# Kernel tuning notes

Measured on AMD Instinct MI355X. Metric: run time of the kernel, lower is better.

## Reference

```python
import jax, jax.numpy as jnp
import numpy as np

B, T = 64, 512
OBS, DM, DS, NL = 115, 128, 8, 3
EMB, NA, H1 = 16, 19, 256


def _ln(x, g, b, eps=1e-5):
    m = jnp.mean(x, -1, keepdims=True)
    v = jnp.mean((x - m) ** 2, -1, keepdims=True)
    return (x - m) * jax.lax.rsqrt(v + eps) * g + b


def _s6(x, h, lng, lnb, w_ig, w_dt, b_dt, a_log, w_b, w_c, d_par, w_out):
    # x: [B,T,DM], h: [B,DM,DS]
    xn = _ln(x, lng, lnb)
    xp = xn @ w_ig.T                               # [B,T,2*DM]
    x_in, z = xp[..., :DM], xp[..., DM:]
    dt = jax.nn.softplus(x_in @ w_dt.T + b_dt)     # [B,T,DM]
    A = -jnp.exp(a_log)                            # [DM,DS]
    bt = x_in @ w_b.T                              # [B,T,DS]
    ct = x_in @ w_c.T                              # [B,T,DS]
    dA = jnp.exp(dt[..., None] * A)                # [B,T,DM,DS]
    upd = (dt * x_in)[..., None] * bt[:, :, None, :]  # [B,T,DM,DS]

    def step(hc, inp):
        dA_t, u_t, c_t = inp
        hn = dA_t * hc + u_t                       # [B,DM,DS]
        y = jnp.einsum('bds,bs->bd', hn, c_t)      # [B,DM]
        return hn, y

    h_f, ys = jax.lax.scan(
        step, h,
        (jnp.swapaxes(dA, 0, 1), jnp.swapaxes(upd, 0, 1), jnp.swapaxes(ct, 0, 1)))
    y = jnp.swapaxes(ys, 0, 1)                     # [B,T,DM]
    ssm = y * jax.nn.silu(z) + x_in * d_par
    return x + ssm @ w_out.T, h_f.reshape(h_f.shape[0], -1)


def _forward(prev_actions, obs, h0, enc_w1, enc_b1, enc_g1, enc_bb1, enc_w2, enc_b2,
             enc_g2, enc_bb2, emb, proj_w, proj_b, proj_g, proj_bb,
             m_ln_g, m_ln_b, m_w_ig, m_w_dt, m_b_dt, m_a_log, m_w_b, m_w_c, m_d, m_w_out,
             fn_g, fn_b, pol_w1, pol_b1, pol_g, pol_bb, pol_w2, pol_b2):
    # MLP encoder: Linear -> LN -> SiLU -> Linear -> LN (final norm)
    e = jax.nn.silu(_ln(obs @ enc_w1.T + enc_b1, enc_g1, enc_bb1))
    e = _ln(e @ enc_w2.T + enc_b2, enc_g2, enc_bb2)
    pa = emb[prev_actions]                         # [B,T,EMB]
    x = jnp.concatenate([e, pa], -1) @ proj_w.T + proj_b
    x = jax.nn.silu(_ln(x, proj_g, proj_bb))
    for i in range(NL):
        x, _ = _s6(x, h0[i].reshape(-1, DM, DS), m_ln_g[i], m_ln_b[i], m_w_ig[i],
                   m_w_dt[i], m_b_dt[i], m_a_log[i], m_w_b[i], m_w_c[i], m_d[i], m_w_out[i])
    x = _ln(x, fn_g, fn_b)
    p = jax.nn.silu(_ln(x @ pol_w1.T + pol_b1, pol_g, pol_bb))
    return p @ pol_w2.T + pol_b2                   # [B,T,NA] policy logits


def setup_inputs() -> dict:
    key = jax.random.key(0)
    ks = iter(jax.random.split(key, 64))
    def n(shape, s=0.05):
        return jax.random.normal(next(ks), shape, dtype=jnp.float32) * s
    return {
        'obs': jax.random.normal(next(ks), (B, T, OBS), dtype=jnp.float32),
        'h0': jnp.zeros((NL, B, DM * DS), jnp.float32),
        'enc_w1': n((H1, OBS)), 'enc_b1': jnp.zeros((H1,)),
        'enc_g1': jnp.ones((H1,)), 'enc_bb1': jnp.zeros((H1,)),
        'enc_w2': n((DM, H1)), 'enc_b2': jnp.zeros((DM,)),
        'enc_g2': jnp.ones((DM,)), 'enc_bb2': jnp.zeros((DM,)),
        'emb': n((NA + 1, EMB), 1.0),
        'proj_w': n((DM, DM + EMB)), 'proj_b': jnp.zeros((DM,)),
        'proj_g': jnp.ones((DM,)), 'proj_bb': jnp.zeros((DM,)),
        'm_ln_g': jnp.ones((NL, DM)), 'm_ln_b': jnp.zeros((NL, DM)),
        'm_w_ig': n((NL, 2 * DM, DM)), 'm_w_dt': n((NL, DM, DM)),
        'm_b_dt': jnp.zeros((NL, DM)),
        'm_a_log': jax.random.uniform(next(ks), (NL, DM, DS), minval=-3.0, maxval=-1.0, dtype=jnp.float32),
        'm_w_b': n((NL, DS, DM)), 'm_w_c': n((NL, DS, DM)),
        'm_d': jnp.ones((NL, DM)), 'm_w_out': n((NL, DM, DM)),
        'fn_g': jnp.ones((DM,)), 'fn_b': jnp.zeros((DM,)),
        'pol_w1': n((DM, DM)), 'pol_b1': jnp.zeros((DM,)),
        'pol_g': jnp.ones((DM,)), 'pol_bb': jnp.zeros((DM,)),
        'pol_w2': n((NA, DM)), 'pol_b2': jnp.zeros((NA,)),
        'prev_actions': jax.random.randint(next(ks), (B, T), 0, NA + 1),
    }


def reference(obs, h0, enc_w1, enc_b1, enc_g1, enc_bb1, enc_w2, enc_b2, enc_g2, enc_bb2,
              emb, proj_w, proj_b, proj_g, proj_bb, m_ln_g, m_ln_b, m_w_ig, m_w_dt,
              m_b_dt, m_a_log, m_w_b, m_w_c, m_d, m_w_out, fn_g, fn_b, pol_w1, pol_b1,
              pol_g, pol_bb, pol_w2, pol_b2, prev_actions):
    return _forward(prev_actions, obs, h0, enc_w1, enc_b1, enc_g1, enc_bb1, enc_w2,
                    enc_b2, enc_g2, enc_bb2, emb, proj_w, proj_b, proj_g, proj_bb,
                    m_ln_g, m_ln_b, m_w_ig, m_w_dt, m_b_dt, m_a_log, m_w_b, m_w_c,
                    m_d, m_w_out, fn_g, fn_b, pol_w1, pol_b1, pol_g, pol_bb, pol_w2, pol_b2)
```

## Files before the change

### kernel.cpp

```cpp
#include <hip/hip_runtime.h>
#include <math.h>

#define BB 64
#define TT 512
#define OBSD 115
#define DMD 128
#define DSD 8
#define NLD 3
#define EMBD 16
#define NAD 19
#define H1D 256
#define NTOK (BB*TT)
#define SSEG 32
#define TSEG (TT/SSEG)

typedef unsigned short ushort_t;
typedef __attribute__((ext_vector_type(8))) short short8;
typedef __attribute__((ext_vector_type(4))) float f32x4;

__device__ __forceinline__ float silu_f(float x){ return x / (1.f + __expf(-x)); }
__device__ __forceinline__ float softplus_f(float x){
  return fmaxf(x, 0.f) + log1pf(__expf(-fabsf(x)));
}
__device__ __forceinline__ ushort_t f2bf(float x){
  unsigned u = __float_as_uint(x);
  unsigned r = (u + 0x7fffu + ((u >> 16) & 1u)) >> 16;
  return (ushort_t)r;
}
__device__ __forceinline__ float b2f(ushort_t x){
  return __uint_as_float(((unsigned)x) << 16);
}
#define MFMA(a,b,c) __builtin_amdgcn_mfma_f32_16x16x32_bf16((a),(b),(c),0,0,0)
#define LOG2E 1.44269504f

template<int D, int SV>
__device__ __forceinline__ void ln32(const float* s_val, float* s_mr, int tid){
  const int t = tid >> 3, part = tid & 7;
  float s = 0.f, s2 = 0.f;
  #pragma unroll
  for (int j = part; j < D; j += 8){ float v = s_val[t*SV + j]; s += v; s2 = fmaf(v, v, s2); }
  s += __shfl_xor(s, 1, 64); s2 += __shfl_xor(s2, 1, 64);
  s += __shfl_xor(s, 2, 64); s2 += __shfl_xor(s2, 2, 64);
  s += __shfl_xor(s, 4, 64); s2 += __shfl_xor(s2, 4, 64);
  if (part == 0){
    float m = s * (1.f/(float)D);
    s_mr[t*2] = m;
    s_mr[t*2+1] = rsqrtf(s2 * (1.f/(float)D) - m*m + 1e-5f);
  }
}

struct PJob { const float* src; ushort_t* dst; int N; int K; int Kpad; int rowofs; int Nw; };
struct PJobs { PJob j[20]; };

__global__ __launch_bounds__(256) void k_prep(PJobs P){
  const int job = blockIdx.x >> 2;
  const int sub = blockIdx.x & 3;
  PJob pj = P.j[job];
  const int elems = pj.Nw * pj.Kpad;
  for (int idx = sub*256 + threadIdx.x; idx < elems; idx += 4*256){
    int n = idx / pj.Kpad;
    int k = idx - n*pj.Kpad;
    float v = (n < pj.N && k < pj.K) ? pj.src[(size_t)n*pj.K + k] : 0.f;
    pj.dst[(size_t)(pj.rowofs + n)*pj.Kpad + k] = f2bf(v);
  }
}

__global__ __launch_bounds__(256) void k_enc12p(
    const float* __restrict__ obs, const ushort_t* __restrict__ w1b,
    const float* __restrict__ b1, const float* __restrict__ g1,
    const float* __restrict__ bb1,
    const ushort_t* __restrict__ w2b,
    const float* __restrict__ b2, const float* __restrict__ g2,
    const float* __restrict__ bb2,
    const float* __restrict__ emb, const int* __restrict__ pact,
    const ushort_t* __restrict__ pwb, const float* __restrict__ pb,
    const float* __restrict__ pg, const float* __restrict__ pbb,
    float* __restrict__ X,
    const float* __restrict__ lng, const float* __restrict__ lnb,
    const ushort_t* __restrict__ wigb, const ushort_t* __restrict__ wdbcb,
    const float* __restrict__ bdt,
    ushort_t* __restrict__ XINb, ushort_t* __restrict__ Zb,
    ushort_t* __restrict__ DTb, ushort_t* __restrict__ BTu, ushort_t* __restrict__ CTu,
    const float* __restrict__ alog0,
    float* __restrict__ HLOC, float* __restrict__ PPR)
{
  __shared__ __align__(16) char sm[35584];
  float*    s_val  = (float*)sm;
  ushort_t* s_obs  = (ushort_t*)sm;
  ushort_t* s_xin  = (ushort_t*)sm;
  ushort_t* s_dt   = (ushort_t*)(sm + 8704);
  ushort_t* s_e1   = (ushort_t*)(sm + 17408);
  ushort_t* s_a2   = (ushort_t*)(sm + 17408);
  float2*   s_st   = (float2*)(sm + 34304);
  ushort_t* s_btc  = (ushort_t*)(sm + 34816);
  float*    s_mr   = (float*)(sm + 35328);

  const int tok0 = blockIdx.x * 32;
  const int bidx = blockIdx.x >> 4;
  const int ch   = blockIdx.x & 15;
  const int tid = threadIdx.x;
  const int lane = tid & 63, w = tid >> 6;
  const int q = lane >> 4, cn = lane & 15;
  const int m0 = (w & 1) * 16, nh = w >> 1;

  for (int e = tid; e < 32*16; e += 256){
    int t = e >> 4, kc = e & 15;
    const float* op = obs + (size_t)(tok0 + t)*OBSD;
    short8 v;
    #pragma unroll
    for (int j = 0; j < 8; j++){
      int k = kc*8 + j;
      v[j] = (short)f2bf(k < OBSD ? op[k] : 0.f);
    }
    *(short8*)&s_obs[t*136 + kc*8] = v;
  }
  __syncthreads();

  f32x4 acc[8];
  {
    short8 af[4];
    #pragma unroll
    for (int ks = 0; ks < 4; ks++)
      af[ks] = *(const short8*)&s_obs[(m0 + cn)*136 + ks*32 + q*8];
    #pragma unroll
    for (int nt = 0; nt < 8; nt++){
      const int n0 = (nh*8 + nt) * 16;
      f32x4 a = {0.f,0.f,0.f,0.f};
      #pragma unroll
      for (int ks = 0; ks < 4; ks++){
        short8 bf = *(const short8*)&w1b[(size_t)(n0 + cn)*128 + ks*32 + q*8];
        a = MFMA(af[ks], bf, a);
      }
      float bv = b1[n0 + cn];
      #pragma unroll
      for (int r = 0; r < 4; r++) a[r] += bv;
      acc[nt] = a;
    }
  }

  {
    #pragma unroll
    for (int r = 0; r < 4; r++){
      float s = 0.f, s2 = 0.f;
      #pragma unroll
      for (int nt = 0; nt < 8; nt++){ float v = acc[nt][r]; s += v; s2 = fmaf(v, v, s2); }
      s += __shfl_xor(s, 1, 64); s2 += __shfl_xor(s2, 1, 64);
      s += __shfl_xor(s, 2, 64); s2 += __shfl_xor(s2, 2, 64);
      s += __shfl_xor(s, 4, 64); s2 += __shfl_xor(s2, 4, 64);
      s += __shfl_xor(s, 8, 64); s2 += __shfl_xor(s2, 8, 64);
      if (cn == 0) s_st[(m0 + q*4 + r)*2 + nh] = make_float2(s, s2);
    }
  }
  __syncthreads();

  {
    float mu[4], rs[4];
    #pragma unroll
    for (int r = 0; r < 4; r++){
      const int row = m0 + q*4 + r;
      float2 p0 = s_st[row*2 + 0], p1 = s_st[row*2 + 1];
      float s = p0.x + p1.x, s2 = p0.y + p1.y;
      float m = s * (1.f/256.f);
      mu[r] = m;
      rs[r] = rsqrtf(s2 * (1.f/256.f) - m*m + 1e-5f);
    }
    #pragma unroll
    for (int nt = 0; nt < 8; nt++){
      const int col = (nh*8 + nt)*16 + cn;
      float gg = g1[col], bbv = bb1[col];
      #pragma unroll
      for (int r = 0; r < 4; r++){
        float v = (acc[nt][r] - mu[r]) * rs[r] * gg + bbv;
        s_e1[(m0 + q*4 + r)*264 + col] = f2bf(silu_f(v));
      }
    }
  }
  __syncthreads();

  {
    short8 af2[8];
    #pragma unroll
    for (int ks = 0; ks < 8; ks++)
      af2[ks] = *(const short8*)&s_e1[(m0 + cn)*264 + ks*32 + q*8];
    __syncthreads();

    for (int e = tid; e < 32*32; e += 256){
      int t = e >> 5, k = e & 31;
      float v = 0.f;
      if (k < EMBD){ int a = pact[tok0 + t]; v = emb[(size_t)a*EMBD + k]; }
      s_a2[t*168 + 128 + k] = f2bf(v);
    }

    #pragma unroll
    for (int nt = 0; nt < 4; nt++){
      const int n0 = (nh*4 + nt) * 16;
      f32x4 a = {0.f,0.f,0.f,0.f};
      #pragma unroll
      for (int ks = 0; ks < 8; ks++){
        short8 bf = *(const short8*)&w2b[(size_t)(n0 + cn)*256 + ks*32 + q*8];
        a = MFMA(af2[ks], bf, a);
      }
      float bias = b2[n0 + cn];
      #pragma unroll
      for (int r = 0; r < 4; r++)
        s_val[(m0 + q*4 + r)*136 + n0 + cn] = a[r] + bias;
    }
  }
  __syncthreads();

  ln32<128,136>(s_val, s_mr, tid);
  __syncthreads();
  for (int e = tid; e < 32*128; e += 256){
    int t = e >> 7, c = e & 127;
    float v = (s_val[t*136 + c] - s_mr[t*2]) * s_mr[t*2+1] * g2[c] + bb2[c];
    s_a2[t*168 + c] = f2bf(v);
  }
  __syncthreads();

  {
    short8 af3[5];
    #pragma unroll
    for (int ks = 0; ks < 5; ks++)
      af3[ks] = *(const short8*)&s_a2[(m0 + cn)*168 + ks*32 + q*8];
    #pragma unroll
    for (int nt = 0; nt < 4; nt++){
      const int n0 = (nh*4 + nt) * 16;
      f32x4 a = {0.f,0.f,0.f,0.f};
      #pragma unroll
      for (int ks = 0; ks < 5; ks++){
        short8 bf = *(const short8*)&pwb[(size_t)(n0 + cn)*160 + ks*32 + q*8];
        a = MFMA(af3[ks], bf, a);
      }
      float bias = pb[n0 + cn];
      #pragma unroll
      for (int r = 0; r < 4; r++)
        s_val[(m0 + q*4 + r)*136 + n0 + cn] = a[r] + bias;
    }
  }
  __syncthreads();

  ln32<128,136>(s_val, s_mr, tid);
  __syncthreads();
  for (int e = tid; e < 32*128; e += 256){
    int t = e >> 7, c = e & 127;
    float v = (s_val[t*136 + c] - s_mr[t*2]) * s_mr[t*2+1] * pg[c] + pbb[c];
    v = silu_f(v);
    X[(size_t)tok0*128 + e] = v;
    s_val[t*136 + c] = v;
  }
  __syncthreads();

  ln32<128,136>(s_val, s_mr, tid);
  __syncthreads();
  for (int e = tid; e < 32*128; e += 256){
    int t = e >> 7, c = e & 127;
    float v = (s_val[t*136 + c] - s_mr[t*2]) * s_mr[t*2+1] * lng[c] + lnb[c];
    s_a2[t*168 + c] = f2bf(v);
  }
  __syncthreads();

  {
    short8 af[4];
    #pragma unroll
    for (int ks = 0; ks < 4; ks++)
      af[ks] = *(const short8*)&s_a2[(m0 + cn)*168 + ks*32 + q*8];
    #pragma unroll
    for (int nt = 0; nt < 8; nt++){
      const int n0 = (nh*8 + nt) * 16;
      f32x4 a = {0.f,0.f,0.f,0.f};
      #pragma unroll
      for (int ks = 0; ks < 4; ks++){
        short8 bf = *(const short8*)&wigb[(size_t)(n0 + cn)*128 + ks*32 + q*8];
        a = MFMA(af[ks], bf, a);
      }
      if (n0 < 128){
        #pragma unroll
        for (int r = 0; r < 4; r++){
          int tr = m0 + q*4 + r;
          ushort_t bb = f2bf(a[r]);
          XINb[(size_t)(tok0 + tr)*128 + n0 + cn] = bb;
          s_xin[tr*136 + n0 + cn] = bb;
        }
      } else {
        #pragma unroll
        for (int r = 0; r < 4; r++){
          int tr = m0 + q*4 + r;
          Zb[(size_t)(tok0 + tr)*128 + (n0 - 128) + cn] = f2bf(a[r]);
        }
      }
    }
  }
  __syncthreads();

  {
    short8 af2[4];
    #pragma unroll
    for (int ks = 0; ks < 4; ks++)
      af2[ks] = *(const short8*)&s_xin[(m0 + cn)*136 + ks*32 + q*8];
    for (int nt = nh; nt < 9; nt += 2){
      const int n0 = nt * 16;
      f32x4 a = {0.f,0.f,0.f,0.f};
      #pragma unroll
      for (int ks = 0; ks < 4; ks++){
        short8 bf = *(const short8*)&wdbcb[(size_t)(n0 + cn)*128 + ks*32 + q*8];
        a = MFMA(af2[ks], bf, a);
      }
      const int col = n0 + cn;
      if (col < 128){
        float bd = bdt[col];
        #pragma unroll
        for (int r = 0; r < 4; r++){
          int tr = m0 + q*4 + r;
          ushort_t dv = f2bf(softplus_f(a[r] + bd));
          DTb[(size_t)(tok0 + tr)*128 + col] = dv;
          s_dt[tr*136 + col] = dv;
        }
      } else if (col < 136){
        #pragma unroll
        for (int r = 0; r < 4; r++){
          int tr = m0 + q*4 + r;
          ushort_t bb = f2bf(a[r]);
          BTu[(size_t)(tok0 + tr)*8 + (col - 128)] = bb;
          s_btc[tr*8 + (col - 128)] = bb;
        }
      } else {
        #pragma unroll
        for (int r = 0; r < 4; r++)
          CTu[(size_t)(tok0 + m0 + q*4 + r)*8 + (col - 136)] = f2bf(a[r]);
      }
    }
  }
  __syncthreads();

  {
    const int d = tid & 127, half = tid >> 7;
    float A2c[8], hh[8], pp[8];
    #pragma unroll
    for (int s = 0; s < 8; s++){
      A2c[s] = -__expf(alog0[d*8 + s]) * LOG2E;
      hh[s] = 0.f; pp[s] = 1.f;
    }
    const int t0 = half * 16;
    #pragma unroll 4
    for (int tt = 0; tt < 16; tt++){
      const int t = t0 + tt;
      float dt = b2f(s_dt[t*136 + d]);
      float wv = dt * b2f(s_xin[t*136 + d]);
      #pragma unroll
      for (int s = 0; s < 8; s++){
        float dA = exp2f(dt * A2c[s]);
        hh[s] = fmaf(dA, hh[s], wv * b2f(s_btc[t*8 + s]));
        pp[s] *= dA;
      }
    }
    const size_t o = ((size_t)bidx*SSEG + ch*2 + half)*1024 + d*8;
    #pragma unroll
    for (int s = 0; s < 8; s++){ HLOC[o+s] = hh[s]; PPR[o+s] = pp[s]; }
  }
}

__global__ __launch_bounds__(256) void k_carry(
    float* __restrict__ HL, const float* __restrict__ PP,
    const float* __restrict__ h0g)
{
  const int idx = blockIdx.x*256 + threadIdx.x;
  const size_t base = (size_t)(idx >> 10) * (SSEG*1024) + (idx & 1023);
  float hl[SSEG], pp[SSEG];
  #pragma unroll
  for (int ch = 0; ch < SSEG; ch++){
    hl[ch] = HL[base + (size_t)ch*1024];
    pp[ch] = PP[base + (size_t)ch*1024];
  }
  float h = h0g[idx];
  #pragma unroll
  for (int ch = 0; ch < SSEG; ch++){
    HL[base + (size_t)ch*1024] = h;
    h = fmaf(pp[ch], h, hl[ch]);
  }
}

#define SMB 26624

__device__ __forceinline__ void phaseB32(
    const ushort_t* DTb, const ushort_t* XINb, const ushort_t* Zb,
    const ushort_t* BTu, const ushort_t* CTu,
    const float* __restrict__ alog, const float* __restrict__ HLpre,
    const float* __restrict__ dpar, const ushort_t* __restrict__ woutb,
    float* __restrict__ X, char* sm, int b, int pair, int tid)
{
  ushort_t* s_dtS = (ushort_t*)sm;
  ushort_t* s_xiS = (ushort_t*)(sm + 8192);
  float*    s_x   = (float*)sm;
  ushort_t* s_a   = (ushort_t*)(sm + 16640);
  ushort_t* s_bt  = (ushort_t*)(sm + 25344);
  ushort_t* s_ct  = (ushort_t*)(sm + 25856);
  float*    s_mr  = (float*)(sm + 26368);

  const int lane = tid & 63, w = tid >> 6, q = lane >> 4, cn = lane & 15;
  const int m0 = (w & 1) * 16, nh = w >> 1;
  const int d = tid & 127, half = tid >> 7;
  const size_t segtok = (size_t)b*TT + pair*32;

  {
    const uint4* gdt = (const uint4*)(DTb + segtok*128);
    const uint4* gxi = (const uint4*)(XINb + segtok*128);
    #pragma unroll
    for (int i = 0; i < 2; i++){
      ((uint4*)s_dtS)[tid + i*256] = gdt[tid + i*256];
      ((uint4*)s_xiS)[tid + i*256] = gxi[tid + i*256];
    }
    if (tid < 128){
      ((unsigned*)s_bt)[tid] = ((const unsigned*)(BTu + segtok*8))[tid];
      ((unsigned*)s_ct)[tid] = ((const unsigned*)(CTu + segtok*8))[tid];
    }
  }
  float A2[8], h[8];
  {
    const size_t o = ((size_t)b*SSEG + pair*2 + half)*1024 + d*8;
    float4 h0v = *(const float4*)(HLpre + o);
    float4 h1v = *(const float4*)(HLpre + o + 4);
    h[0]=h0v.x; h[1]=h0v.y; h[2]=h0v.z; h[3]=h0v.w;
    h[4]=h1v.x; h[5]=h1v.y; h[6]=h1v.z; h[7]=h1v.w;
    #pragma unroll
    for (int s = 0; s < 8; s++) A2[s] = -__expf(alog[d*8 + s]) * LOG2E;
  }
  __syncthreads();

  #pragma unroll 4
  for (int tt = 0; tt < 16; tt++){
    const int t = half*16 + tt;
    float dt = b2f(s_dtS[t*128 + d]);
    float xi = b2f(s_xiS[t*128 + d]);
    float wv = dt * xi;
    float y = 0.f;
    #pragma unroll
    for (int s = 0; s < 8; s++){
      float dA = exp2f(dt * A2[s]);
      h[s] = fmaf(dA, h[s], wv * b2f(s_bt[t*8 + s]));
      y = fmaf(h[s], b2f(s_ct[t*8 + s]), y);
    }
    s_a[t*136 + d] = f2bf(y);
  }
  __syncthreads();

  {
    const int c0 = (tid & 15)*8, trow = tid >> 4;
    float dpv[8];
    #pragma unroll
    for (int j = 0; j < 8; j++) dpv[j] = dpar[c0 + j];
    #pragma unroll
    for (int i = 0; i < 2; i++){
      const int t = trow + i*16;
      uint4 zb = ((const uint4*)(Zb + segtok*128))[tid + i*256];
      const ushort_t* zp = (const ushort_t*)&zb;
      #pragma unroll
      for (int j = 0; j < 8; j++){
        float y  = b2f(s_a[t*136 + c0 + j]);
        float xi = b2f(s_xiS[t*128 + c0 + j]);
        float ssm = y * silu_f(b2f(zp[j])) + xi * dpv[j];
        s_a[t*136 + c0 + j] = f2bf(ssm);
      }
    }
  }
  __syncthreads();

  {
    short8 af[4];
    #pragma unroll
    for (int ks = 0; ks < 4; ks++)
      af[ks] = *(const short8*)&s_a[(m0 + cn)*136 + ks*32 + q*8];
    #pragma unroll
    for (int i = 0; i < 4; i++){
      const int n0 = (nh*4 + i) * 16;
      short8 bf[4];
      #pragma unroll
      for (int ks = 0; ks < 4; ks++)
        bf[ks] = *(const short8*)&woutb[(size_t)(n0+cn)*128 + ks*32 + q*8];
      f32x4 acc = {0.f,0.f,0.f,0.f};
      #pragma unroll
      for (int ks = 0; ks < 4; ks++) acc = MFMA(af[ks], bf[ks], acc);
      #pragma unroll
      for (int r = 0; r < 4; r++){
        const int tr = m0 + q*4 + r;
        const size_t g = (segtok + tr)*128 + n0 + cn;
        float xn = X[g] + acc[r];
        X[g] = xn;
        s_x[tr*130 + n0 + cn] = xn;
      }
    }
  }
  __syncthreads();

  {
    const int t = tid >> 3, part = tid & 7;
    float s = 0.f, s2 = 0.f;
    const float* row = s_x + t*130 + part*16;
    #pragma unroll
    for (int j = 0; j < 16; j++){ float v = row[j]; s += v; s2 = fmaf(v, v, s2); }
    s  += __shfl_xor(s, 1, 64);  s2 += __shfl_xor(s2, 1, 64);
    s  += __shfl_xor(s, 2, 64);  s2 += __shfl_xor(s2, 2, 64);
    s  += __shfl_xor(s, 4, 64);  s2 += __shfl_xor(s2, 4, 64);
    if (part == 0){
      float m = s * (1.f/128.f);
      s_mr[t*2] = m;
      s_mr[t*2+1] = rsqrtf(s2 * (1.f/128.f) - m*m + 1e-5f);
    }
  }
  __syncthreads();
}

__global__ __launch_bounds__(256, 4) void k_scan2p(
    ushort_t* DTb, ushort_t* XINb, ushort_t* Zb,
    ushort_t* BTu, ushort_t* CTu,
    const float* __restrict__ alog, const float* __restrict__ HLpre,
    const float* __restrict__ dpar, const ushort_t* __restrict__ woutb,
    float* __restrict__ X,
    const float* __restrict__ lng, const float* __restrict__ lnb,
    const ushort_t* __restrict__ wigb, const ushort_t* __restrict__ wdbcb,
    const float* __restrict__ bdt,
    const float* __restrict__ alogn,
    float* __restrict__ HLo, float* __restrict__ PPo)
{
  __shared__ __align__(16) char sm[SMB];
  const int tid = threadIdx.x;
  float*    s_x   = (float*)sm;
  ushort_t* s_xin = (ushort_t*)sm;
  ushort_t* s_dt2 = (ushort_t*)(sm + 8704);
  ushort_t* s_a   = (ushort_t*)(sm + 16640);
  ushort_t* s_btc = (ushort_t*)(sm + 25344);
  float*    s_mr  = (float*)(sm + 26368);

  const int b = blockIdx.x >> 4;
  const int pair = blockIdx.x & 15;
  const int lane = tid & 63, w = tid >> 6, q = lane >> 4, cn = lane & 15;
  const int m0 = (w & 1) * 16, nh = w >> 1;
  const int d = tid & 127, half = tid >> 7;
  const size_t segtok = (size_t)b*TT + pair*32;

  phaseB32(DTb, XINb, Zb, BTu, CTu, alog, HLpre, dpar, woutb, X, sm, b, pair, tid);

  {
    float g = lng[d], c0v = lnb[d];
    #pragma unroll
    for (int tt = 0; tt < 16; tt++){
      const int t = half*16 + tt;
      float v = (s_x[t*130 + d] - s_mr[t*2]) * s_mr[t*2+1] * g + c0v;
      s_a[t*136 + d] = f2bf(v);
    }
  }
  __syncthreads();

  {
    short8 af[4];
    #pragma unroll
    for (int ks = 0; ks < 4; ks++)
      af[ks] = *(const short8*)&s_a[(m0 + cn)*136 + ks*32 + q*8];
    #pragma unroll
    for (int i = 0; i < 8; i++){
      const int n0 = (nh*8 + i) * 16;
      short8 bf[4];
      #pragma unroll
      for (int ks = 0; ks < 4; ks++)
        bf[ks] = *(const short8*)&wigb[(size_t)(n0+cn)*128 + ks*32 + q*8];
      f32x4 acc = {0.f,0.f,0.f,0.f};
      #pragma unroll
      for (int ks = 0; ks < 4; ks++) acc = MFMA(af[ks], bf[ks], acc);
      if (n0 < 128){
        #pragma unroll
        for (int r = 0; r < 4; r++){
          const int tr = m0 + q*4 + r;
          ushort_t bb = f2bf(acc[r]);
          XINb[(segtok + tr)*128 + n0 + cn] = bb;
          s_xin[tr*136 + n0 + cn] = bb;
        }
      } else {
        #pragma unroll
        for (int r = 0; r < 4; r++){
          const int tr = m0 + q*4 + r;
          Zb[(segtok + tr)*128 + (n0-128) + cn] = f2bf(acc[r]);
        }
      }
    }
  }
  __syncthreads();

  {
    short8 af2[4];
    #pragma unroll
    for (int ks = 0; ks < 4; ks++)
      af2[ks] = *(const short8*)&s_xin[(m0 + cn)*136 + ks*32 + q*8];
    for (int nt = nh; nt < 9; nt += 2){
      const int n0 = nt * 16;
      short8 bf[4];
      #pragma unroll
      for (int ks = 0; ks < 4; ks++)
        bf[ks] = *(const short8*)&wdbcb[(size_t)(n0+cn)*128 + ks*32 + q*8];
      f32x4 acc = {0.f,0.f,0.f,0.f};
      #pragma unroll
      for (int ks = 0; ks < 4; ks++) acc = MFMA(af2[ks], bf[ks], acc);
      const int col = n0 + cn;
      if (col < 128){
        float bd = bdt[col];
        #pragma unroll
        for (int r = 0; r < 4; r++){
          const int tr = m0 + q*4 + r;
          ushort_t dv = f2bf(softplus_f(acc[r] + bd));
          DTb[(segtok + tr)*128 + col] = dv;
          s_dt2[tr*136 + col] = dv;
        }
      } else if (col < 136){
        #pragma unroll
        for (int r = 0; r < 4; r++){
          const int tr = m0 + q*4 + r;
          ushort_t bb = f2bf(acc[r]);
          BTu[(segtok + tr)*8 + (col-128)] = bb;
          s_btc[tr*8 + (col-128)] = bb;
        }
      } else {
        #pragma unroll
        for (int r = 0; r < 4; r++)
          CTu[(segtok + m0 + q*4 + r)*8 + (col-136)] = f2bf(acc[r]);
      }
    }
  }
  __syncthreads();

  {
    float A2n[8], hh[8], pp[8];
    #pragma unroll
    for (int s = 0; s < 8; s++){
      A2n[s] = -__expf(alogn[d*8 + s]) * LOG2E;
      hh[s] = 0.f; pp[s] = 1.f;
    }
    #pragma unroll 4
    for (int tt = 0; tt < 16; tt++){
      const int t = half*16 + tt;
      float dt = b2f(s_dt2[t*136 + d]);
      float wv = dt * b2f(s_xin[t*136 + d]);
      #pragma unroll
      for (int s = 0; s < 8; s++){
        float dA = exp2f(dt * A2n[s]);
        hh[s] = fmaf(dA, hh[s], wv * b2f(s_btc[t*8 + s]));
        pp[s] *= dA;
      }
    }
    const size_t o = ((size_t)b*SSEG + pair*2 + half)*1024 + d*8;
    #pragma unroll
    for (int s = 0; s < 8; s++){ HLo[o+s] = hh[s]; PPo[o+s] = pp[s]; }
  }
}

__global__ __launch_bounds__(256, 4) void k_scan2h(
    const ushort_t* DTb, const ushort_t* XINb, const ushort_t* Zb,
    const ushort_t* BTu, const ushort_t* CTu,
    const float* __restrict__ alog, const float* __restrict__ HLpre,
    const float* __restrict__ dpar, const ushort_t* __restrict__ woutb,
    float* __restrict__ X,
    const float* __restrict__ fng, const float* __restrict__ fnb,
    const ushort_t* __restrict__ pw1b, const float* __restrict__ pb1,
    const float* __restrict__ pg, const float* __restrict__ pbb,
    const ushort_t* __restrict__ pw2b, const float* __restrict__ pb2,
    float* __restrict__ out)
{
  __shared__ __align__(16) char sm[SMB];
  const int tid = threadIdx.x;
  float*    s_x  = (float*)sm;
  ushort_t* s_a  = (ushort_t*)(sm + 16640);
  float*    s_mr = (float*)(sm + 26368);

  const int b = blockIdx.x >> 4;
  const int pair = blockIdx.x & 15;
  const int lane = tid & 63, w = tid >> 6, q = lane >> 4, cn = lane & 15;
  const int m0 = (w & 1) * 16, nh = w >> 1;
  const int d = tid & 127, half = tid >> 7;
  const size_t segtok = (size_t)b*TT + pair*32;

  phaseB32((ushort_t*)DTb, (ushort_t*)XINb, (ushort_t*)Zb,
           (ushort_t*)BTu, (ushort_t*)CTu, alog, HLpre,
           dpar, woutb, X, sm, b, pair, tid);

  {
    float g = fng[d], c0v = fnb[d];
    #pragma unroll
    for (int tt = 0; tt < 16; tt++){
      const int t = half*16 + tt;
      float v = (s_x[t*130 + d] - s_mr[t*2]) * s_mr[t*2+1] * g + c0v;
      s_a[t*136 + d] = f2bf(v);
    }
  }
  __syncthreads();

  {
    short8 af[4];
    #pragma unroll
    for (int ks = 0; ks < 4; ks++)
      af[ks] = *(const short8*)&s_a[(m0 + cn)*136 + ks*32 + q*8];
    #pragma unroll
    for (int i = 0; i < 4; i++){
      const int n0 = (nh*4 + i) * 16;
      short8 bf[4];
      #pragma unroll
      for (int ks = 0; ks < 4; ks++)
        bf[ks] = *(const short8*)&pw1b[(size_t)(n0+cn)*128 + ks*32 + q*8];
      float bias = pb1[n0 + cn];
      f32x4 acc = {0.f,0.f,0.f,0.f};
      #pragma unroll
      for (int ks = 0; ks < 4; ks++) acc = MFMA(af[ks], bf[ks], acc);
      #pragma unroll
      for (int r = 0; r < 4; r++)
        s_x[(m0 + q*4 + r)*130 + n0 + cn] = acc[r] + bias;
    }
  }
  __syncthreads();

  {
    const int t = tid >> 3, part = tid & 7;
    float s = 0.f, s2 = 0.f;
    const float* row = s_x + t*130 + part*16;
    #pragma unroll
    for (int j = 0; j < 16; j++){ float v = row[j]; s += v; s2 = fmaf(v, v, s2); }
    s  += __shfl_xor(s, 1, 64);  s2 += __shfl_xor(s2, 1, 64);
    s  += __shfl_xor(s, 2, 64);  s2 += __shfl_xor(s2, 2, 64);
    s  += __shfl_xor(s, 4, 64);  s2 += __shfl_xor(s2, 4, 64);
    if (part == 0){
      float m = s * (1.f/128.f);
      s_mr[t*2] = m;
      s_mr[t*2+1] = rsqrtf(s2 * (1.f/128.f) - m*m + 1e-5f);
    }
  }
  __syncthreads();

  {
    float g = pg[d], c0v = pbb[d];
    #pragma unroll
    for (int tt = 0; tt < 16; tt++){
      const int t = half*16 + tt;
      float v = (s_x[t*130 + d] - s_mr[t*2]) * s_mr[t*2+1] * g + c0v;
      s_a[t*136 + d] = f2bf(silu_f(v));
    }
  }
  __syncthreads();

  {
    short8 af[4];
    #pragma unroll
    for (int ks = 0; ks < 4; ks++)
      af[ks] = *(const short8*)&s_a[(m0 + cn)*136 + ks*32 + q*8];
    const int n0 = (w >> 1) * 16;
    short8 bf[4];
    #pragma unroll
    for (int ks = 0; ks < 4; ks++)
      bf[ks] = *(const short8*)&pw2b[(size_t)(n0+cn)*128 + ks*32 + q*8];
    const int col = n0 + cn;
    f32x4 acc = {0.f,0.f,0.f,0.f};
    #pragma unroll
    for (int ks = 0; ks < 4; ks++) acc = MFMA(af[ks], bf[ks], acc);
    if (col < NAD){
      float bias = pb2[col];
      #pragma unroll
      for (int r = 0; r < 4; r++)
        out[(segtok + m0 + q*4 + r)*NAD + col] = acc[r] + bias;
    }
  }
}

extern "C" void kernel_launch(void* const* d_in, const int* in_sizes, int n_in,
                              void* d_out, int out_size, void* d_ws, size_t ws_size,
                              hipStream_t stream) {
  const float* obs    = (const float*)d_in[0];
  const float* h0     = (const float*)d_in[1];
  const float* enc_w1 = (const float*)d_in[2];
  const float* enc_b1 = (const float*)d_in[3];
  const float* enc_g1 = (const float*)d_in[4];
  const float* enc_bb1= (const float*)d_in[5];
  const float* enc_w2 = (const float*)d_in[6];
  const float* enc_b2 = (const float*)d_in[7];
  const float* enc_g2 = (const float*)d_in[8];
  const float* enc_bb2= (const float*)d_in[9];
  const float* emb    = (const float*)d_in[10];
  const float* proj_w = (const float*)d_in[11];
  const float* proj_b = (const float*)d_in[12];
  const float* proj_g = (const float*)d_in[13];
  const float* proj_bb= (const float*)d_in[14];
  const float* m_ln_g = (const float*)d_in[15];
  const float* m_ln_b = (const float*)d_in[16];
  const float* m_w_ig = (const float*)d_in[17];
  const float* m_w_dt = (const float*)d_in[18];
  const float* m_b_dt = (const float*)d_in[19];
  const float* m_a_log= (const float*)d_in[20];
  const float* m_w_b  = (const float*)d_in[21];
  const float* m_w_c  = (const float*)d_in[22];
  const float* m_d    = (const float*)d_in[23];
  const float* m_w_out= (const float*)d_in[24];
  const float* fn_g   = (const float*)d_in[25];
  const float* fn_b   = (const float*)d_in[26];
  const float* pol_w1 = (const float*)d_in[27];
  const float* pol_b1 = (const float*)d_in[28];
  const float* pol_g  = (const float*)d_in[29];
  const float* pol_bb = (const float*)d_in[30];
  const float* pol_w2 = (const float*)d_in[31];
  const float* pol_b2 = (const float*)d_in[32];
  const int*   pact   = (const int*)d_in[33];

  float* ws  = (float*)d_ws;
  float* X    = ws;
  float* HLA  = X + (size_t)NTOK*128;
  float* PPA  = HLA + (size_t)BB*SSEG*1024;
  float* HLB  = PPA + (size_t)BB*SSEG*1024;
  float* PPB  = HLB + (size_t)BB*SSEG*1024;
  ushort_t* XINb = (ushort_t*)(PPB + (size_t)BB*SSEG*1024);
  ushort_t* Zb   = XINb + (size_t)NTOK*128;
  ushort_t* DTb  = Zb   + (size_t)NTOK*128;
  ushort_t* BTu  = DTb  + (size_t)NTOK*128;
  ushort_t* CTu  = BTu  + (size_t)NTOK*8;

  ushort_t* W1B   = CTu   + (size_t)NTOK*8;
  ushort_t* W2B   = W1B   + 256*128;
  ushort_t* PWB   = W2B   + 128*256;
  ushort_t* WIGB  = PWB   + 128*160;
  ushort_t* WDBCB = WIGB  + 3*256*128;
  ushort_t* WOUTB = WDBCB + 3*144*128;
  ushort_t* PW1B  = WOUTB + 3*128*128;
  ushort_t* PW2B  = PW1B  + 128*128;

  PJobs P;
  int nj = 0;
  auto add = [&](const float* src, ushort_t* dst, int N, int K, int Kpad, int rowofs, int Nw){
    P.j[nj].src = src; P.j[nj].dst = dst; P.j[nj].N = N; P.j[nj].K = K;
    P.j[nj].Kpad = Kpad; P.j[nj].rowofs = rowofs; P.j[nj].Nw = Nw; nj++;
  };
  add(enc_w1, W1B, 256, 115, 128, 0, 256);
  add(enc_w2, W2B, 128, 256, 256, 0, 128);
  add(proj_w, PWB, 128, 144, 160, 0, 128);
  for (int l = 0; l < NLD; l++)
    add(m_w_ig + (size_t)l*256*128, WIGB + (size_t)l*256*128, 256, 128, 128, 0, 256);
  for (int l = 0; l < NLD; l++){
    add(m_w_dt + (size_t)l*128*128, WDBCB + (size_t)l*144*128, 128, 128, 128, 0,   128);
    add(m_w_b  + (size_t)l*8*128,   WDBCB + (size_t)l*144*128,   8, 128, 128, 128,   8);
    add(m_w_c  + (size_t)l*8*128,   WDBCB + (size_t)l*144*128,   8, 128, 128, 136,   8);
  }
  for (int l = 0; l < NLD; l++)
    add(m_w_out + (size_t)l*128*128, WOUTB + (size_t)l*128*128, 128, 128, 128, 0, 128);
  add(pol_w1, PW1B, 128, 128, 128, 0, 128);
  add(pol_w2, PW2B,  19, 128, 128, 0,  32);

  k_prep<<<20*4, 256, 0, stream>>>(P);
  k_enc12p<<<NTOK/32, 256, 0, stream>>>(obs, W1B, enc_b1, enc_g1, enc_bb1,
      W2B, enc_b2, enc_g2, enc_bb2,
      emb, pact, PWB, proj_b, proj_g, proj_bb, X,
      m_ln_g, m_ln_b, WIGB, WDBCB, m_b_dt,
      XINb, Zb, DTb, BTu, CTu,
      m_a_log, HLA, PPA);

  const int carrygrid = BB*1024/256;
  const int scangrid  = NTOK/32;

  k_carry<<<carrygrid, 256, 0, stream>>>(HLA, PPA, h0);
  k_scan2p<<<scangrid, 256, 0, stream>>>(DTb, XINb, Zb, BTu, CTu,
      m_a_log, HLA, m_d, WOUTB, X,
      m_ln_g + 128, m_ln_b + 128,
      WIGB + (size_t)256*128, WDBCB + (size_t)144*128, m_b_dt + 128,
      m_a_log + 1024, HLB, PPB);
  k_carry<<<carrygrid, 256, 0, stream>>>(HLB, PPB, h0 + (size_t)BB*1024);
  k_scan2p<<<scangrid, 256, 0, stream>>>(DTb, XINb, Zb, BTu, CTu,
      m_a_log + 1024, HLB, m_d + 128, WOUTB + (size_t)128*128, X,
      m_ln_g + 256, m_ln_b + 256,
      WIGB + (size_t)2*256*128, WDBCB + (size_t)2*144*128, m_b_dt + 256,
      m_a_log + 2048, HLA, PPA);
  k_carry<<<carrygrid, 256, 0, stream>>>(HLA, PPA, h0 + (size_t)2*BB*1024);
  k_scan2h<<<scangrid, 256, 0, stream>>>(DTb, XINb, Zb, BTu, CTu,
      m_a_log + 2048, HLA, m_d + 256, WOUTB + (size_t)2*128*128, X,
      fn_g, fn_b, PW1B, pol_b1, pol_g, pol_bb, PW2B, pol_b2,
      (float*)d_out);
}
```

Before: 409.0 us.

## Fuse LayerNorm statistics into MFMA epilogues and merge SSM gating into scan

LayerNorm mean/variance is now reduced from the MFMA accumulator registers with lane shuffles and cross-wave partials in shared memory. This replaces the separate shared-memory store, reduce pass and normalize pass, removing several barriers and LDS round trips in the encoder and scan kernels. The z gate and D-skip are now applied inside the scan loop, with z preloaded into shared memory, instead of in a separate pass that re-read y and x_in. In exchange the shared-memory footprint of the scan kernels grows, which may lower occupancy, and the encoder gets a launch-bounds occupancy hint.

```diff
diff --git a/kernel.cpp b/kernel.cpp
--- a/kernel.cpp
+++ b/kernel.cpp
@@ -33,22 +33,6 @@
 #define MFMA(a,b,c) __builtin_amdgcn_mfma_f32_16x16x32_bf16((a),(b),(c),0,0,0)
 #define LOG2E 1.44269504f
 
-template<int D, int SV>
-__device__ __forceinline__ void ln32(const float* s_val, float* s_mr, int tid){
-  const int t = tid >> 3, part = tid & 7;
-  float s = 0.f, s2 = 0.f;
-  #pragma unroll
-  for (int j = part; j < D; j += 8){ float v = s_val[t*SV + j]; s += v; s2 = fmaf(v, v, s2); }
-  s += __shfl_xor(s, 1, 64); s2 += __shfl_xor(s2, 1, 64);
-  s += __shfl_xor(s, 2, 64); s2 += __shfl_xor(s2, 2, 64);
-  s += __shfl_xor(s, 4, 64); s2 += __shfl_xor(s2, 4, 64);
-  if (part == 0){
-    float m = s * (1.f/(float)D);
-    s_mr[t*2] = m;
-    s_mr[t*2+1] = rsqrtf(s2 * (1.f/(float)D) - m*m + 1e-5f);
-  }
-}
-
 struct PJob { const float* src; ushort_t* dst; int N; int K; int Kpad; int rowofs; int Nw; };
 struct PJobs { PJob j[20]; };
 
@@ -65,7 +49,7 @@
   }
 }
 
-__global__ __launch_bounds__(256) void k_enc12p(
+__global__ __launch_bounds__(256, 4) void k_enc12p(
     const float* __restrict__ obs, const ushort_t* __restrict__ w1b,
     const float* __restrict__ b1, const float* __restrict__ g1,
     const float* __restrict__ bb1,
@@ -84,16 +68,15 @@
     const float* __restrict__ alog0,
     float* __restrict__ HLOC, float* __restrict__ PPR)
 {
-  __shared__ __align__(16) char sm[35584];
-  float*    s_val  = (float*)sm;
+  __shared__ __align__(16) char sm[29184];
   ushort_t* s_obs  = (ushort_t*)sm;
+  ushort_t* s_e1   = (ushort_t*)sm;
   ushort_t* s_xin  = (ushort_t*)sm;
   ushort_t* s_dt   = (ushort_t*)(sm + 8704);
-  ushort_t* s_e1   = (ushort_t*)(sm + 17408);
-  ushort_t* s_a2   = (ushort_t*)(sm + 17408);
-  float2*   s_st   = (float2*)(sm + 34304);
-  ushort_t* s_btc  = (ushort_t*)(sm + 34816);
-  float*    s_mr   = (float*)(sm + 35328);
+  ushort_t* s_a2   = (ushort_t*)(sm + 16896);
+  ushort_t* s_btc  = (ushort_t*)(sm + 27648);
+  float2*   s_st   = (float2*)(sm + 28160);
+  float2*   s_st2  = (float2*)(sm + 28672);
 
   const int tok0 = blockIdx.x * 32;
   const int bidx = blockIdx.x >> 4;
@@ -114,6 +97,12 @@
     }
     *(short8*)&s_obs[t*136 + kc*8] = v;
   }
+  for (int e = tid; e < 32*32; e += 256){
+    int t = e >> 5, k = e & 31;
+    float v = 0.f;
+    if (k < EMBD){ int a = pact[tok0 + t]; v = emb[(size_t)a*EMBD + k]; }
+    s_a2[t*168 + 128 + k] = f2bf(v);
+  }
   __syncthreads();
 
   f32x4 acc[8];
@@ -136,9 +125,6 @@
       for (int r = 0; r < 4; r++) a[r] += bv;
       acc[nt] = a;
     }
-  }
-
-  {
     #pragma unroll
     for (int r = 0; r < 4; r++){
       float s = 0.f, s2 = 0.f;
@@ -177,20 +163,12 @@
   }
   __syncthreads();
 
+  f32x4 acc2[4];
   {
     short8 af2[8];
     #pragma unroll
     for (int ks = 0; ks < 8; ks++)
       af2[ks] = *(const short8*)&s_e1[(m0 + cn)*264 + ks*32 + q*8];
-    __syncthreads();
-
-    for (int e = tid; e < 32*32; e += 256){
-      int t = e >> 5, k = e & 31;
-      float v = 0.f;
-      if (k < EMBD){ int a = pact[tok0 + t]; v = emb[(size_t)a*EMBD + k]; }
-      s_a2[t*168 + 128 + k] = f2bf(v);
-    }
-
     #pragma unroll
     for (int nt = 0; nt < 4; nt++){
       const int n0 = (nh*4 + nt) * 16;
@@ -200,23 +178,50 @@
         short8 bf = *(const short8*)&w2b[(size_t)(n0 + cn)*256 + ks*32 + q*8];
         a = MFMA(af2[ks], bf, a);
       }
-      float bias = b2[n0 + cn];
-      #pragma unroll
-      for (int r = 0; r < 4; r++)
-        s_val[(m0 + q*4 + r)*136 + n0 + cn] = a[r] + bias;
-    }
-  }
-  __syncthreads();
-
-  ln32<128,136>(s_val, s_mr, tid);
-  __syncthreads();
-  for (int e = tid; e < 32*128; e += 256){
-    int t = e >> 7, c = e & 127;
-    float v = (s_val[t*136 + c] - s_mr[t*2]) * s_mr[t*2+1] * g2[c] + bb2[c];
-    s_a2[t*168 + c] = f2bf(v);
-  }
-  __syncthreads();
-
+      float bv = b2[n0 + cn];
+      #pragma unroll
+      for (int r = 0; r < 4; r++) a[r] += bv;
+      acc2[nt] = a;
+    }
+    #pragma unroll
+    for (int r = 0; r < 4; r++){
+      float s = 0.f, s2 = 0.f;
+      #pragma unroll
+      for (int nt = 0; nt < 4; nt++){ float v = acc2[nt][r]; s += v; s2 = fmaf(v, v, s2); }
+      s += __shfl_xor(s, 1, 64); s2 += __shfl_xor(s2, 1, 64);
+      s += __shfl_xor(s, 2, 64); s2 += __shfl_xor(s2, 2, 64);
+      s += __shfl_xor(s, 4, 64); s2 += __shfl_xor(s2, 4, 64);
+      s += __shfl_xor(s, 8, 64); s2 += __shfl_xor(s2, 8, 64);
+      if (cn == 0) s_st[(m0 + q*4 + r)*2 + nh] = make_float2(s, s2);
+    }
+  }
+  __syncthreads();
+
+  {
+    float mu[4], rs[4];
+    #pragma unroll
+    for (int r = 0; r < 4; r++){
+      const int row = m0 + q*4 + r;
+      float2 p0 = s_st[row*2 + 0], p1 = s_st[row*2 + 1];
+      float s = p0.x + p1.x, s2 = p0.y + p1.y;
+      float m = s * (1.f/128.f);
+      mu[r] = m;
+      rs[r] = rsqrtf(s2 * (1.f/128.f) - m*m + 1e-5f);
+    }
+    #pragma unroll
+    for (int nt = 0; nt < 4; nt++){
+      const int col = (nh*4 + nt)*16 + cn;
+      float gg = g2[col], bbv = bb2[col];
+      #pragma unroll
+      for (int r = 0; r < 4; r++){
+        float v = (acc2[nt][r] - mu[r]) * rs[r] * gg + bbv;
+        s_a2[(m0 + q*4 + r)*168 + col] = f2bf(v);
+      }
+    }
+  }
+  __syncthreads();
+
+  f32x4 acc3[4];
   {
     short8 af3[5];
     #pragma unroll
@@ -231,31 +236,83 @@
         short8 bf = *(const short8*)&pwb[(size_t)(n0 + cn)*160 + ks*32 + q*8];
         a = MFMA(af3[ks], bf, a);
       }
-      float bias = pb[n0 + cn];
-      #pragma unroll
-      for (int r = 0; r < 4; r++)
-        s_val[(m0 + q*4 + r)*136 + n0 + cn] = a[r] + bias;
-    }
-  }
-  __syncthreads();
-
-  ln32<128,136>(s_val, s_mr, tid);
-  __syncthreads();
-  for (int e = tid; e < 32*128; e += 256){
-    int t = e >> 7, c = e & 127;
-    float v = (s_val[t*136 + c] - s_mr[t*2]) * s_mr[t*2+1] * pg[c] + pbb[c];
-    v = silu_f(v);
-    X[(size_t)tok0*128 + e] = v;
-    s_val[t*136 + c] = v;
-  }
-  __syncthreads();
-
-  ln32<128,136>(s_val, s_mr, tid);
-  __syncthreads();
-  for (int e = tid; e < 32*128; e += 256){
-    int t = e >> 7, c = e & 127;
-    float v = (s_val[t*136 + c] - s_mr[t*2]) * s_mr[t*2+1] * lng[c] + lnb[c];
-    s_a2[t*168 + c] = f2bf(v);
+      float bv = pb[n0 + cn];
+      #pragma unroll
+      for (int r = 0; r < 4; r++) a[r] += bv;
+      acc3[nt] = a;
+    }
+    #pragma unroll
+    for (int r = 0; r < 4; r++){
+      float s = 0.f, s2 = 0.f;
+      #pragma unroll
+      for (int nt = 0; nt < 4; nt++){ float v = acc3[nt][r]; s += v; s2 = fmaf(v, v, s2); }
+      s += __shfl_xor(s, 1, 64); s2 += __shfl_xor(s2, 1, 64);
+      s += __shfl_xor(s, 2, 64); s2 += __shfl_xor(s2, 2, 64);
+      s += __shfl_xor(s, 4, 64); s2 += __shfl_xor(s2, 4, 64);
+      s += __shfl_xor(s, 8, 64); s2 += __shfl_xor(s2, 8, 64);
+      if (cn == 0) s_st[(m0 + q*4 + r)*2 + nh] = make_float2(s, s2);
+    }
+  }
+  __syncthreads();
+
+  {
+    float mu[4], rs[4];
+    #pragma unroll
+    for (int r = 0; r < 4; r++){
+      const int row = m0 + q*4 + r;
+      float2 p0 = s_st[row*2 + 0], p1 = s_st[row*2 + 1];
+      float s = p0.x + p1.x, s2 = p0.y + p1.y;
+      float m = s * (1.f/128.f);
+      mu[r] = m;
+      rs[r] = rsqrtf(s2 * (1.f/128.f) - m*m + 1e-5f);
+    }
+    float ps[4] = {0.f,0.f,0.f,0.f}, ps2[4] = {0.f,0.f,0.f,0.f};
+    #pragma unroll
+    for (int nt = 0; nt < 4; nt++){
+      const int col = (nh*4 + nt)*16 + cn;
+      float gg = pg[col], bbv = pbb[col];
+      #pragma unroll
+      for (int r = 0; r < 4; r++){
+        float v = (acc3[nt][r] - mu[r]) * rs[r] * gg + bbv;
+        v = silu_f(v);
+        acc3[nt][r] = v;
+        X[(size_t)(tok0 + m0 + q*4 + r)*128 + col] = v;
+        ps[r] += v; ps2[r] = fmaf(v, v, ps2[r]);
+      }
+    }
+    #pragma unroll
+    for (int r = 0; r < 4; r++){
+      float s = ps[r], s2 = ps2[r];
+      s += __shfl_xor(s, 1, 64); s2 += __shfl_xor(s2, 1, 64);
+      s += __shfl_xor(s, 2, 64); s2 += __shfl_xor(s2, 2, 64);
+      s += __shfl_xor(s, 4, 64); s2 += __shfl_xor(s2, 4, 64);
+      s += __shfl_xor(s, 8, 64); s2 += __shfl_xor(s2, 8, 64);
+      if (cn == 0) s_st2[(m0 + q*4 + r)*2 + nh] = make_float2(s, s2);
+    }
+  }
+  __syncthreads();
+
+  {
+    float mu[4], rs[4];
+    #pragma unroll
+    for (int r = 0; r < 4; r++){
+      const int row = m0 + q*4 + r;
+      float2 p0 = s_st2[row*2 + 0], p1 = s_st2[row*2 + 1];
+      float s = p0.x + p1.x, s2 = p0.y + p1.y;
+      float m = s * (1.f/128.f);
+      mu[r] = m;
+      rs[r] = rsqrtf(s2 * (1.f/128.f) - m*m + 1e-5f);
+    }
+    #pragma unroll
+    for (int nt = 0; nt < 4; nt++){
+      const int col = (nh*4 + nt)*16 + cn;
+      float gg = lng[col], bbv = lnb[col];
+      #pragma unroll
+      for (int r = 0; r < 4; r++){
+        float v = (acc3[nt][r] - mu[r]) * rs[r] * gg + bbv;
+        s_a2[(m0 + q*4 + r)*168 + col] = f2bf(v);
+      }
+    }
   }
   __syncthreads();
 
@@ -379,7 +436,7 @@
   }
 }
 
-#define SMB 26624
+#define SMB 34816
 
 __device__ __forceinline__ void phaseB32(
     const ushort_t* DTb, const ushort_t* XINb, const ushort_t* Zb,
@@ -390,11 +447,12 @@
 {
   ushort_t* s_dtS = (ushort_t*)sm;
   ushort_t* s_xiS = (ushort_t*)(sm + 8192);
+  ushort_t* s_zS  = (ushort_t*)(sm + 16384);
   float*    s_x   = (float*)sm;
-  ushort_t* s_a   = (ushort_t*)(sm + 16640);
-  ushort_t* s_bt  = (ushort_t*)(sm + 25344);
-  ushort_t* s_ct  = (ushort_t*)(sm + 25856);
-  float*    s_mr  = (float*)(sm + 26368);
+  ushort_t* s_a   = (ushort_t*)(sm + 24576);
+  ushort_t* s_bt  = (ushort_t*)(sm + 33280);
+  ushort_t* s_ct  = (ushort_t*)(sm + 33792);
+  float2*   s_st  = (float2*)(sm + 34304);
 
   const int lane = tid & 63, w = tid >> 6, q = lane >> 4, cn = lane & 15;
   const int m0 = (w & 1) * 16, nh = w >> 1;
@@ -404,10 +462,12 @@
   {
     const uint4* gdt = (const uint4*)(DTb + segtok*128);
     const uint4* gxi = (const uint4*)(XINb + segtok*128);
+    const uint4* gz  = (const uint4*)(Zb + segtok*128);
     #pragma unroll
     for (int i = 0; i < 2; i++){
       ((uint4*)s_dtS)[tid + i*256] = gdt[tid + i*256];
       ((uint4*)s_xiS)[tid + i*256] = gxi[tid + i*256];
+      ((uint4*)s_zS )[tid + i*256] = gz [tid + i*256];
     }
     if (tid < 128){
       ((unsigned*)s_bt)[tid] = ((const unsigned*)(BTu + segtok*8))[tid];
@@ -415,6 +475,7 @@
     }
   }
   float A2[8], h[8];
+  float dp = dpar[d];
   {
     const size_t o = ((size_t)b*SSEG + pair*2 + half)*1024 + d*8;
     float4 h0v = *(const float4*)(HLpre + o);
@@ -431,6 +492,7 @@
     const int t = half*16 + tt;
     float dt = b2f(s_dtS[t*128 + d]);
     float xi = b2f(s_xiS[t*128 + d]);
+    float zv = b2f(s_zS [t*128 + d]);
     float wv = dt * xi;
     float y = 0.f;
     #pragma unroll
@@ -439,28 +501,8 @@
       h[s] = fmaf(dA, h[s], wv * b2f(s_bt[t*8 + s]));
       y = fmaf(h[s], b2f(s_ct[t*8 + s]), y);
     }
-    s_a[t*136 + d] = f2bf(y);
-  }
-  __syncthreads();
-
-  {
-    const int c0 = (tid & 15)*8, trow = tid >> 4;
-    float dpv[8];
-    #pragma unroll
-    for (int j = 0; j < 8; j++) dpv[j] = dpar[c0 + j];
-    #pragma unroll
-    for (int i = 0; i < 2; i++){
-      const int t = trow + i*16;
-      uint4 zb = ((const uint4*)(Zb + segtok*128))[tid + i*256];
-      const ushort_t* zp = (const ushort_t*)&zb;
-      #pragma unroll
-      for (int j = 0; j < 8; j++){
-        float y  = b2f(s_a[t*136 + c0 + j]);
-        float xi = b2f(s_xiS[t*128 + c0 + j]);
-        float ssm = y * silu_f(b2f(zp[j])) + xi * dpv[j];
-        s_a[t*136 + c0 + j] = f2bf(ssm);
-      }
-    }
+    float ssm = y * silu_f(zv) + xi * dp;
+    s_a[t*136 + d] = f2bf(ssm);
   }
   __syncthreads();
 
@@ -469,6 +511,7 @@
     #pragma unroll
     for (int ks = 0; ks < 4; ks++)
       af[ks] = *(const short8*)&s_a[(m0 + cn)*136 + ks*32 + q*8];
+    float ps[4] = {0.f,0.f,0.f,0.f}, ps2[4] = {0.f,0.f,0.f,0.f};
     #pragma unroll
     for (int i = 0; i < 4; i++){
       const int n0 = (nh*4 + i) * 16;
@@ -486,24 +529,17 @@
         float xn = X[g] + acc[r];
         X[g] = xn;
         s_x[tr*130 + n0 + cn] = xn;
-      }
-    }
-  }
-  __syncthreads();
-
-  {
-    const int t = tid >> 3, part = tid & 7;
-    float s = 0.f, s2 = 0.f;
-    const float* row = s_x + t*130 + part*16;
-    #pragma unroll
-    for (int j = 0; j < 16; j++){ float v = row[j]; s += v; s2 = fmaf(v, v, s2); }
-    s  += __shfl_xor(s, 1, 64);  s2 += __shfl_xor(s2, 1, 64);
-    s  += __shfl_xor(s, 2, 64);  s2 += __shfl_xor(s2, 2, 64);
-    s  += __shfl_xor(s, 4, 64);  s2 += __shfl_xor(s2, 4, 64);
-    if (part == 0){
-      float m = s * (1.f/128.f);
-      s_mr[t*2] = m;
-      s_mr[t*2+1] = rsqrtf(s2 * (1.f/128.f) - m*m + 1e-5f);
+        ps[r] += xn; ps2[r] = fmaf(xn, xn, ps2[r]);
+      }
+    }
+    #pragma unroll
+    for (int r = 0; r < 4; r++){
+      float s = ps[r], s2 = ps2[r];
+      s += __shfl_xor(s, 1, 64); s2 += __shfl_xor(s2, 1, 64);
+      s += __shfl_xor(s, 2, 64); s2 += __shfl_xor(s2, 2, 64);
+      s += __shfl_xor(s, 4, 64); s2 += __shfl_xor(s2, 4, 64);
+      s += __shfl_xor(s, 8, 64); s2 += __shfl_xor(s2, 8, 64);
+      if (cn == 0) s_st[(m0 + q*4 + r)*2 + nh] = make_float2(s, s2);
     }
   }
   __syncthreads();
@@ -526,9 +562,9 @@
   float*    s_x   = (float*)sm;
   ushort_t* s_xin = (ushort_t*)sm;
   ushort_t* s_dt2 = (ushort_t*)(sm + 8704);
-  ushort_t* s_a   = (ushort_t*)(sm + 16640);
-  ushort_t* s_btc = (ushort_t*)(sm + 25344);
-  float*    s_mr  = (float*)(sm + 26368);
+  ushort_t* s_a   = (ushort_t*)(sm + 24576);
+  ushort_t* s_btc = (ushort_t*)(sm + 33280);
+  float2*   s_st  = (float2*)(sm + 34304);
 
   const int b = blockIdx.x >> 4;
   const int pair = blockIdx.x & 15;
@@ -544,7 +580,11 @@
     #pragma unroll
     for (int tt = 0; tt < 16; tt++){
       const int t = half*16 + tt;
-      float v = (s_x[t*130 + d] - s_mr[t*2]) * s_mr[t*2+1] * g + c0v;
+      float2 p0 = s_st[t*2 + 0], p1 = s_st[t*2 + 1];
+      float ssum = p0.x + p1.x, ss2 = p0.y + p1.y;
+      float mu = ssum * (1.f/128.f);
+      float rs = rsqrtf(ss2 * (1.f/128.f) - mu*mu + 1e-5f);
+      float v = (s_x[t*130 + d] - mu) * rs * g + c0v;
       s_a[t*136 + d] = f2bf(v);
     }
   }
@@ -665,8 +705,8 @@
   __shared__ __align__(16) char sm[SMB];
   const int tid = threadIdx.x;
   float*    s_x  = (float*)sm;
-  ushort_t* s_a  = (ushort_t*)(sm + 16640);
-  float*    s_mr = (float*)(sm + 26368);
+  ushort_t* s_a  = (ushort_t*)(sm + 24576);
+  float2*   s_st = (float2*)(sm + 34304);
 
   const int b = blockIdx.x >> 4;
   const int pair = blockIdx.x & 15;
@@ -684,7 +724,11 @@
     #pragma unroll
     for (int tt = 0; tt < 16; tt++){
       const int t = half*16 + tt;
-      float v = (s_x[t*130 + d] - s_mr[t*2]) * s_mr[t*2+1] * g + c0v;
+      float2 p0 = s_st[t*2 + 0], p1 = s_st[t*2 + 1];
+      float ssum = p0.x + p1.x, ss2 = p0.y + p1.y;
+      float mu = ssum * (1.f/128.f);
+      float rs = rsqrtf(ss2 * (1.f/128.f) - mu*mu + 1e-5f);
+      float v = (s_x[t*130 + d] - mu) * rs * g + c0v;
       s_a[t*136 + d] = f2bf(v);
     }
   }
@@ -695,6 +739,7 @@
     #pragma unroll
     for (int ks = 0; ks < 4; ks++)
       af[ks] = *(const short8*)&s_a[(m0 + cn)*136 + ks*32 + q*8];
+    float ps[4] = {0.f,0.f,0.f,0.f}, ps2[4] = {0.f,0.f,0.f,0.f};
     #pragma unroll
     for (int i = 0; i < 4; i++){
       const int n0 = (nh*4 + i) * 16;
@@ -707,25 +752,20 @@
       #pragma unroll
       for (int ks = 0; ks < 4; ks++) acc = MFMA(af[ks], bf[ks], acc);
       #pragma unroll
-      for (int r = 0; r < 4; r++)
-        s_x[(m0 + q*4 + r)*130 + n0 + cn] = acc[r] + bias;
-    }
-  }
-  __syncthreads();
-
-  {
-    const int t = tid >> 3, part = tid & 7;
-    float s = 0.f, s2 = 0.f;
-    const float* row = s_x + t*130 + part*16;
-    #pragma unroll
-    for (int j = 0; j < 16; j++){ float v = row[j]; s += v; s2 = fmaf(v, v, s2); }
-    s  += __shfl_xor(s, 1, 64);  s2 += __shfl_xor(s2, 1, 64);
-    s  += __shfl_xor(s, 2, 64);  s2 += __shfl_xor(s2, 2, 64);
-    s  += __shfl_xor(s, 4, 64);  s2 += __shfl_xor(s2, 4, 64);
-    if (part == 0){
-      float m = s * (1.f/128.f);
-      s_mr[t*2] = m;
-      s_mr[t*2+1] = rsqrtf(s2 * (1.f/128.f) - m*m + 1e-5f);
+      for (int r = 0; r < 4; r++){
+        float xv = acc[r] + bias;
+        s_x[(m0 + q*4 + r)*130 + n0 + cn] = xv;
+        ps[r] += xv; ps2[r] = fmaf(xv, xv, ps2[r]);
+      }
+    }
+    #pragma unroll
+    for (int r = 0; r < 4; r++){
+      float s = ps[r], s2 = ps2[r];
+      s += __shfl_xor(s, 1, 64); s2 += __shfl_xor(s2, 1, 64);
+      s += __shfl_xor(s, 2, 64); s2 += __shfl_xor(s2, 2, 64);
+      s += __shfl_xor(s, 4, 64); s2 += __shfl_xor(s2, 4, 64);
+      s += __shfl_xor(s, 8, 64); s2 += __shfl_xor(s2, 8, 64);
+      if (cn == 0) s_st[(m0 + q*4 + r)*2 + nh] = make_float2(s, s2);
     }
   }
   __syncthreads();
@@ -735,7 +775,11 @@
     #pragma unroll
     for (int tt = 0; tt < 16; tt++){
       const int t = half*16 + tt;
-      float v = (s_x[t*130 + d] - s_mr[t*2]) * s_mr[t*2+1] * g + c0v;
+      float2 p0 = s_st[t*2 + 0], p1 = s_st[t*2 + 1];
+      float ssum = p0.x + p1.x, ss2 = p0.y + p1.y;
+      float mu = ssum * (1.f/128.f);
+      float rs = rsqrtf(ss2 * (1.f/128.f) - mu*mu + 1e-5f);
+      float v = (s_x[t*130 + d] - mu) * rs * g + c0v;
       s_a[t*136 + d] = f2bf(silu_f(v));
     }
   }
```

Measured after the change: 407.0 us. Within noise of the previous version (-0.5%).
